# Optimization experiments

Hardware: AMD Instinct MI355X
Metric: run time of the kernel (lower is better)

Reference implementation:

```python
import jax, jax.numpy as jnp
import numpy as np

EPS = 1e-8

def rms_norm(x, scale):
    # norm(2,-1)/sqrt(d); x / (rms + eps) * scale
    d = x.shape[-1]
    norm = jnp.sqrt(jnp.sum(x * x, axis=-1, keepdims=True))
    rms = norm / jnp.sqrt(jnp.asarray(d, x.dtype))
    return scale * (x / (rms + EPS))

def setup_inputs() -> dict:
    key = jax.random.key(0)
    B, N, C, FF = 2, 2048, 1024, 4096
    ks = jax.random.split(key, 12)
    s = 0.02
    return {
        "x":  jax.random.normal(ks[0], (B, N, C), jnp.float32),
        "wq": jax.random.normal(ks[1], (C, C), jnp.float32) * s,
        "bq": jnp.zeros((C,), jnp.float32),
        "wk": jax.random.normal(ks[2], (C, C), jnp.float32) * s,
        "bk": jnp.zeros((C,), jnp.float32),
        "wv": jax.random.normal(ks[3], (C, C), jnp.float32) * s,
        "bv": jnp.zeros((C,), jnp.float32),
        "wo": jax.random.normal(ks[4], (C, C), jnp.float32) * s,
        "bo": jnp.zeros((C,), jnp.float32),
        "scale1": jnp.ones((C,), jnp.float32),
        "scale2": jnp.ones((C,), jnp.float32),
        "w1": jax.random.normal(ks[5], (C, FF), jnp.float32) * s,
        "b1": jnp.zeros((FF,), jnp.float32),
        "w2": jax.random.normal(ks[6], (FF, C), jnp.float32) * s,
        "b2": jnp.zeros((C,), jnp.float32),
    }

def reference(x, wq, bq, wk, bk, wv, bv, wo, bo, scale1, scale2, w1, b1, w2, b2):
    B, N, C = x.shape
    H = 16
    D = C // H

    residual = x
    xn = rms_norm(x, scale1)

    def heads(y):  # [B,N,C] -> [B,H,N,D]
        return y.reshape(B, N, H, D).transpose(0, 2, 1, 3)

    q = heads(xn @ wq + bq)
    k = heads(xn @ wk + bk)
    v = heads(xn @ wv + bv)

    # apply_rotary_pos_emb with cos=sin=1: q' = q - roll(q,1,-1), same for k
    q = q - jnp.roll(q, 1, axis=-1)
    k = k - jnp.roll(k, 1, axis=-1)

    # explicit attention (no causal mask in original)
    scores = jnp.einsum('bhnd,bhmd->bhnm', q, k) / jnp.sqrt(jnp.asarray(D, x.dtype))
    probs = jax.nn.softmax(scores, axis=-1)
    attn = jnp.einsum('bhnm,bhmd->bhnd', probs, v)
    attn = attn.transpose(0, 2, 1, 3).reshape(B, N, C)
    attn = attn @ wo + bo

    x = residual + attn
    residual = x
    xn = rms_norm(x, scale2)
    h = jax.nn.gelu(xn @ w1 + b1, approximate=False)  # torch GELU default = exact
    ffn_out = h @ w2 + b2
    return residual + ffn_out
```

## Files before the change

kernel.cpp:

```cpp
#include <hip/hip_runtime.h>
#include <hip/hip_bf16.h>
#include <math.h>

typedef unsigned short u16;
typedef short s16x8 __attribute__((ext_vector_type(8)));
typedef __bf16 bf16x8v __attribute__((ext_vector_type(8)));
typedef float f32x4 __attribute__((ext_vector_type(4)));
typedef unsigned short u16x4 __attribute__((ext_vector_type(4)));

struct Ptr4 { float* p[4]; };
struct TW4 { const float* w[4]; u16* o[4]; };

__device__ __forceinline__ u16 f2b(float f) {
    __hip_bfloat16 h = __float2bfloat16(f);
    return __builtin_bit_cast(u16, h);
}
__device__ __forceinline__ float b2f(u16 u) {
    __hip_bfloat16 h = __builtin_bit_cast(__hip_bfloat16, u);
    return __bfloat162float(h);
}

__device__ __forceinline__ f32x4 mfma16(s16x8 a, s16x8 b, f32x4 c) {
    return __builtin_amdgcn_mfma_f32_16x16x32_bf16(
        __builtin_bit_cast(bf16x8v, a), __builtin_bit_cast(bf16x8v, b), c, 0, 0, 0);
}

__device__ __forceinline__ void gl_lds16(const void* g, void* l) {
    typedef const unsigned int __attribute__((address_space(1))) * gp_t;
    typedef unsigned int __attribute__((address_space(3))) * lp_t;
    __builtin_amdgcn_global_load_lds((gp_t)(unsigned long long)g,
                                     (lp_t)(unsigned int)(unsigned long long)l,
                                     16, 0, 0);
}

__device__ __forceinline__ float gelu_fast(float v) {
    float u = 1.5957691216f * (v + 0.044715f * v * v * v);
    return v / (1.f + __expf(-u));
}

__global__ __launch_bounds__(256) void transpose_w(const float* __restrict__ W,
                                                   u16* __restrict__ Wt,
                                                   int K, int N) {
    __shared__ u16 tile[32][33];
    const int tx = threadIdx.x & 31, ty = threadIdx.x >> 5;
    const int n0 = blockIdx.x * 32, k0 = blockIdx.y * 32;
#pragma unroll
    for (int i = 0; i < 32; i += 8)
        tile[ty + i][tx] = f2b(W[(size_t)(k0 + ty + i) * N + n0 + tx]);
    __syncthreads();
#pragma unroll
    for (int i = 0; i < 32; i += 8)
        Wt[(size_t)(n0 + ty + i) * K + k0 + tx] = tile[tx][ty + i];
}

__global__ __launch_bounds__(256) void transpose_w4(TW4 io) {
    __shared__ u16 tile[32][33];
    const int z = blockIdx.z;
    const float* W = io.w[z];
    u16* Wt = io.o[z];
    const int tx = threadIdx.x & 31, ty = threadIdx.x >> 5;
    const int n0 = blockIdx.x * 32, k0 = blockIdx.y * 32;
#pragma unroll
    for (int i = 0; i < 32; i += 8)
        tile[ty + i][tx] = f2b(W[(size_t)(k0 + ty + i) * 1024 + n0 + tx]);
    __syncthreads();
#pragma unroll
    for (int i = 0; i < 32; i += 8)
        Wt[(size_t)(n0 + ty + i) * 1024 + k0 + tx] = tile[tx][ty + i];
}

__global__ __launch_bounds__(256) void transpose_v(const u16* __restrict__ qkv,
                                                   u16* __restrict__ vT) {
    __shared__ u16 tile[32][33];
    const int tx = threadIdx.x & 31, ty = threadIdx.x >> 5;
    const int n0 = blockIdx.x * 32, d0 = blockIdx.y * 32, bh = blockIdx.z;
    const int b = bh >> 4, h = bh & 15;
#pragma unroll
    for (int i = 0; i < 32; i += 8)
        tile[ty + i][tx] =
            qkv[(size_t)(b * 2048 + n0 + ty + i) * 3072 + 2048 + h * 64 + d0 + tx];
    __syncthreads();
#pragma unroll
    for (int i = 0; i < 32; i += 8)
        vT[((size_t)bh * 64 + d0 + ty + i) * 2048 + n0 + tx] = tile[tx][ty + i];
}

__global__ __launch_bounds__(256) void rmsnorm_kernel(const float* __restrict__ x,
                                                      const float* __restrict__ scale,
                                                      u16* __restrict__ out) {
    __shared__ float red[4];
    const int t = threadIdx.x, row = blockIdx.x;
    const float4* xr = (const float4*)(x + (size_t)row * 1024);
    float4 v = xr[t];
    float ss = v.x * v.x + v.y * v.y + v.z * v.z + v.w * v.w;
#pragma unroll
    for (int off = 1; off < 64; off <<= 1) ss += __shfl_xor(ss, off);
    if ((t & 63) == 0) red[t >> 6] = ss;
    __syncthreads();
    float tot = red[0] + red[1] + red[2] + red[3];
    float inv = 1.f / (sqrtf(tot * (1.f / 1024.f)) + 1e-8f);
    const float4* sr = (const float4*)scale;
    float4 s = sr[t];
    u16x4 o;
    o[0] = f2b(v.x * inv * s.x);
    o[1] = f2b(v.y * inv * s.y);
    o[2] = f2b(v.z * inv * s.z);
    o[3] = f2b(v.w * inv * s.w);
    ((u16x4*)(out + (size_t)row * 1024))[t] = o;
}

template <int EPI>
__global__ __launch_bounds__(256) void gemm_kernel(const u16* __restrict__ A,
                                                   const u16* __restrict__ Bt,
                                                   const float* __restrict__ bias,
                                                   const float* __restrict__ bias2,
                                                   const float* __restrict__ bias3,
                                                   const float* __restrict__ resid,
                                                   void* __restrict__ outp,
                                                   int M, int N, int K) {
    __shared__ __align__(16) u16 As[128 * 32];
    __shared__ __align__(16) u16 Bs[128 * 32];
    const int t = threadIdx.x, lane = t & 63;
    const int w = t >> 6, wm = (w >> 1) * 64, wn = (w & 1) * 64;
    const int c = lane & 15, qd = lane >> 4;
    const int n0 = blockIdx.x * 128, m0 = blockIdx.y * 128;

    const int sch = ((t & 3) ^ ((t >> 3) & 3)) * 8;
    const u16* Ag = A + (size_t)(m0 + (t >> 2)) * K + sch;
    const u16* Bg = Bt + (size_t)(n0 + (t >> 2)) * K + sch;
    const size_t half = (size_t)64 * K;
    const int fsw = ((c >> 1) & 3);

    f32x4 acc[4][4] = {};
    for (int kt = 0; kt < K; kt += 32) {
        __syncthreads();
        gl_lds16(Ag, &As[t * 8]);
        gl_lds16(Ag + half, &As[2048 + t * 8]);
        gl_lds16(Bg, &Bs[t * 8]);
        gl_lds16(Bg + half, &Bs[2048 + t * 8]);
        Ag += 32;
        Bg += 32;
        __syncthreads();
        s16x8 a[4], b[4];
#pragma unroll
        for (int im = 0; im < 4; im++)
            a[im] = *(const s16x8*)&As[(wm + im * 16 + c) * 32 + ((qd ^ fsw) * 8)];
#pragma unroll
        for (int jn = 0; jn < 4; jn++)
            b[jn] = *(const s16x8*)&Bs[(wn + jn * 16 + c) * 32 + ((qd ^ fsw) * 8)];
#pragma unroll
        for (int im = 0; im < 4; im++)
#pragma unroll
            for (int jn = 0; jn < 4; jn++)
                acc[im][jn] = mfma16(a[im], b[jn], acc[im][jn]);
    }

    if (EPI == 3) {
        const int colbase = n0 + wn;
        const bool isq = colbase < 1024, isv = colbase >= 2048;
        const float* bp = isq ? bias : (isv ? bias3 : bias2);
        const int cb = colbase & 1023;
#pragma unroll
        for (int im = 0; im < 4; im++)
#pragma unroll
            for (int r = 0; r < 4; r++) {
                float v[4], sh[4], b15[4];
#pragma unroll
                for (int jn = 0; jn < 4; jn++)
                    v[jn] = acc[im][jn][r] + bp[cb + jn * 16 + c];
#pragma unroll
                for (int jn = 0; jn < 4; jn++) {
                    sh[jn] = __shfl(v[jn], qd * 16 + ((c + 15) & 15));
                    b15[jn] = __shfl(v[jn], qd * 16 + 15);
                }
                const int rowg = m0 + wm + im * 16 + qd * 4 + r;
#pragma unroll
                for (int jn = 0; jn < 4; jn++) {
                    float prev = (c == 0) ? b15[(jn + 3) & 3] : sh[jn];
                    float ov = isv ? v[jn] : (v[jn] - prev);
                    if (isq) ov *= 0.125f;
                    ((u16*)outp)[(size_t)rowg * N + colbase + jn * 16 + c] = f2b(ov);
                }
            }
        return;
    }

#pragma unroll
    for (int im = 0; im < 4; im++) {
#pragma unroll
        for (int jn = 0; jn < 4; jn++) {
            const int colg = n0 + wn + jn * 16 + c;
            const float bv = bias[colg];
#pragma unroll
            for (int r = 0; r < 4; r++) {
                const int rowg = m0 + wm + im * 16 + qd * 4 + r;
                const size_t off = (size_t)rowg * N + colg;
                float v = acc[im][jn][r] + bv;
                if (EPI == 0) {
                    ((u16*)outp)[off] = f2b(v);
                } else if (EPI == 1) {
                    ((float*)outp)[off] = v + resid[off];
                } else {
                    ((u16*)outp)[off] = f2b(gelu_fast(v));
                }
            }
        }
    }
}

__global__ __launch_bounds__(256) void gemm_splitk(const u16* __restrict__ A,
                                                   const u16* __restrict__ Bt,
                                                   Ptr4 parts,
                                                   int N, int Ktot, int Kc) {
    __shared__ __align__(16) u16 As[128 * 32];
    __shared__ __align__(16) u16 Bs[128 * 32];
    const int t = threadIdx.x, lane = t & 63;
    const int w = t >> 6, wm = (w >> 1) * 64, wn = (w & 1) * 64;
    const int c = lane & 15, qd = lane >> 4;
    const int n0 = blockIdx.x * 128, m0 = blockIdx.y * 128;
    const int z = blockIdx.z;
    float* out = parts.p[z];

    const int sch = ((t & 3) ^ ((t >> 3) & 3)) * 8;
    const u16* Ag = A + (size_t)(m0 + (t >> 2)) * Ktot + z * Kc + sch;
    const u16* Bg = Bt + (size_t)(n0 + (t >> 2)) * Ktot + z * Kc + sch;
    const size_t half = (size_t)64 * Ktot;
    const int fsw = ((c >> 1) & 3);

    f32x4 acc[4][4] = {};
    for (int kt = 0; kt < Kc; kt += 32) {
        __syncthreads();
        gl_lds16(Ag, &As[t * 8]);
        gl_lds16(Ag + half, &As[2048 + t * 8]);
        gl_lds16(Bg, &Bs[t * 8]);
        gl_lds16(Bg + half, &Bs[2048 + t * 8]);
        Ag += 32;
        Bg += 32;
        __syncthreads();
        s16x8 a[4], b[4];
#pragma unroll
        for (int im = 0; im < 4; im++)
            a[im] = *(const s16x8*)&As[(wm + im * 16 + c) * 32 + ((qd ^ fsw) * 8)];
#pragma unroll
        for (int jn = 0; jn < 4; jn++)
            b[jn] = *(const s16x8*)&Bs[(wn + jn * 16 + c) * 32 + ((qd ^ fsw) * 8)];
#pragma unroll
        for (int im = 0; im < 4; im++)
#pragma unroll
            for (int jn = 0; jn < 4; jn++)
                acc[im][jn] = mfma16(a[im], b[jn], acc[im][jn]);
    }

#pragma unroll
    for (int im = 0; im < 4; im++)
#pragma unroll
        for (int jn = 0; jn < 4; jn++) {
            const int colg = n0 + wn + jn * 16 + c;
#pragma unroll
            for (int r = 0; r < 4; r++) {
                const int rowg = m0 + wm + im * 16 + qd * 4 + r;
                out[(size_t)rowg * N + colg] = acc[im][jn][r];
            }
        }
}

template <int S, bool NORM>
__global__ __launch_bounds__(256) void reduce_kernel(Ptr4 parts,
                                                     const float* __restrict__ bias,
                                                     const float* __restrict__ resid,
                                                     const float* __restrict__ scale,
                                                     float* __restrict__ yout,
                                                     u16* __restrict__ xnout) {
    __shared__ float red[4];
    const int t = threadIdx.x, row = blockIdx.x;
    const size_t base = (size_t)row * 1024;
    float4 v = ((const float4*)(resid + base))[t];
    float4 bv = ((const float4*)bias)[t];
    v.x += bv.x; v.y += bv.y; v.z += bv.z; v.w += bv.w;
#pragma unroll
    for (int s = 0; s < S; s++) {
        float4 pv = ((const float4*)(parts.p[s] + base))[t];
        v.x += pv.x; v.y += pv.y; v.z += pv.z; v.w += pv.w;
    }
    ((float4*)(yout + base))[t] = v;
    if (NORM) {
        float ss = v.x * v.x + v.y * v.y + v.z * v.z + v.w * v.w;
#pragma unroll
        for (int off = 1; off < 64; off <<= 1) ss += __shfl_xor(ss, off);
        if ((t & 63) == 0) red[t >> 6] = ss;
        __syncthreads();
        float tot = red[0] + red[1] + red[2] + red[3];
        float inv = 1.f / (sqrtf(tot * (1.f / 1024.f)) + 1e-8f);
        float4 s = ((const float4*)scale)[t];
        u16x4 o;
        o[0] = f2b(v.x * inv * s.x);
        o[1] = f2b(v.y * inv * s.y);
        o[2] = f2b(v.z * inv * s.z);
        o[3] = f2b(v.w * inv * s.w);
        ((u16x4*)(xnout + base))[t] = o;
    }
}

__global__ __launch_bounds__(256) void attn_kernel(const u16* __restrict__ qkv,
                                                   const u16* __restrict__ vT,
                                                   u16* __restrict__ attn) {
    __shared__ __align__(16) u16 Qs[64 * 64];
    __shared__ __align__(16) u16 Ks[2][64 * 64];
    __shared__ __align__(16) u16 Vs[2][64 * 64];
    __shared__ __align__(16) u16 Ps[4 * 16 * 64];

    const int t = threadIdx.x, lane = t & 63, w = t >> 6;
    const int c = lane & 15, qd = lane >> 4;
    const int bh = blockIdx.y, b = bh >> 4, h = bh & 15;
    const int q0 = blockIdx.x * 64;
    const size_t rowbase = (size_t)b * 2048;

    const u16* qg = qkv + (rowbase + q0) * 3072 + h * 64;
    const u16* kg = qkv + rowbase * 3072 + 1024 + h * 64;
    const u16* vg = vT + (size_t)bh * 64 * 2048;

    const int srow = t >> 3;
    const int sch = (t & 7) ^ (srow & 7);

    const u16* kptr = kg + (size_t)srow * 3072 + sch * 8;
    const u16* vptr = vg + (size_t)srow * 2048 + sch * 8;

    gl_lds16(qg + (size_t)srow * 3072 + sch * 8, &Qs[t * 8]);
    gl_lds16(qg + (size_t)(srow + 32) * 3072 + sch * 8, &Qs[2048 + t * 8]);
    gl_lds16(kptr, &Ks[0][t * 8]);
    gl_lds16(kptr + (size_t)32 * 3072, &Ks[0][2048 + t * 8]);
    gl_lds16(vptr, &Vs[0][t * 8]);
    gl_lds16(vptr + (size_t)32 * 2048, &Vs[0][2048 + t * 8]);
    __syncthreads();

    const int qrow = w * 16 + c;
    s16x8 qf[2];
#pragma unroll
    for (int ks = 0; ks < 2; ks++)
        qf[ks] = *(const s16x8*)&Qs[qrow * 64 + (((ks * 4 + qd) ^ (c & 7)) * 8)];

    float lsum[4] = {0.f, 0.f, 0.f, 0.f};
    f32x4 o[4] = {};
    u16* Pw = &Ps[w * 16 * 64];

    for (int it = 0; it < 32; it++) {
        const int buf = it & 1;
        const u16* Kb = Ks[buf];
        const u16* Vb = Vs[buf];

        s16x8 kf[2][4], vf[2][4];
#pragma unroll
        for (int ks = 0; ks < 2; ks++)
#pragma unroll
            for (int j = 0; j < 4; j++) {
                const int rrow = j * 16 + c;
                const int sw = ((ks * 4 + qd) ^ (rrow & 7)) * 8;
                kf[ks][j] = *(const s16x8*)&Kb[rrow * 64 + sw];
                vf[ks][j] = *(const s16x8*)&Vb[rrow * 64 + sw];
            }

        if (it + 1 < 32) {
            u16* Kn = Ks[buf ^ 1];
            u16* Vn = Vs[buf ^ 1];
            const size_t ko = (size_t)(it + 1) * 64 * 3072;
            const size_t vo = (size_t)(it + 1) * 64;
            gl_lds16(kptr + ko, &Kn[t * 8]);
            gl_lds16(kptr + ko + (size_t)32 * 3072, &Kn[2048 + t * 8]);
            gl_lds16(vptr + vo, &Vn[t * 8]);
            gl_lds16(vptr + vo + (size_t)32 * 2048, &Vn[2048 + t * 8]);
        }

        f32x4 sc[4] = {};
#pragma unroll
        for (int ks = 0; ks < 2; ks++)
#pragma unroll
            for (int jn = 0; jn < 4; jn++)
                sc[jn] = mfma16(qf[ks], kf[ks][jn], sc[jn]);

#pragma unroll
        for (int r = 0; r < 4; r++) {
            const int prow = qd * 4 + r;
            float s = 0.f;
#pragma unroll
            for (int jn = 0; jn < 4; jn++) {
                float p = __expf(sc[jn][r]);
                s += p;
                Pw[prow * 64 + (((jn * 2 + (c >> 3)) ^ (prow & 7)) * 8) + (c & 7)] =
                    f2b(p);
            }
            lsum[r] += s;
        }

#pragma unroll
        for (int ks = 0; ks < 2; ks++) {
            s16x8 pf = *(const s16x8*)&Pw[c * 64 + (((ks * 4 + qd) ^ (c & 7)) * 8)];
#pragma unroll
            for (int jd = 0; jd < 4; jd++)
                o[jd] = mfma16(pf, vf[ks][jd], o[jd]);
        }
        __syncthreads();
    }

#pragma unroll
    for (int r = 0; r < 4; r++)
#pragma unroll
        for (int off2 = 1; off2 < 16; off2 <<= 1)
            lsum[r] += __shfl_xor(lsum[r], off2);

    const int orow_base = b * 2048 + q0 + w * 16;
#pragma unroll
    for (int r = 0; r < 4; r++) {
        const float inv = 1.f / lsum[r];
        const int grow = orow_base + qd * 4 + r;
#pragma unroll
        for (int jd = 0; jd < 4; jd++)
            attn[(size_t)grow * 1024 + h * 64 + jd * 16 + c] = f2b(o[jd][r] * inv);
    }
}

extern "C" void kernel_launch(void* const* d_in, const int* in_sizes, int n_in,
                              void* d_out, int out_size, void* d_ws, size_t ws_size,
                              hipStream_t stream) {
    const float* x = (const float*)d_in[0];
    const float* wq = (const float*)d_in[1];
    const float* bq = (const float*)d_in[2];
    const float* wk = (const float*)d_in[3];
    const float* bk = (const float*)d_in[4];
    const float* wv = (const float*)d_in[5];
    const float* bv = (const float*)d_in[6];
    const float* wo = (const float*)d_in[7];
    const float* bo = (const float*)d_in[8];
    const float* scale1 = (const float*)d_in[9];
    const float* scale2 = (const float*)d_in[10];
    const float* w1 = (const float*)d_in[11];
    const float* b1 = (const float*)d_in[12];
    const float* w2 = (const float*)d_in[13];
    const float* b2 = (const float*)d_in[14];
    float* out = (float*)d_out;

    char* ws = (char*)d_ws;
    size_t off = 0;
    auto alloc = [&](size_t bytes) -> char* {
        char* p = ws + off;
        off += (bytes + 255) & ~(size_t)255;
        return p;
    };
    u16* wqkvT = (u16*)alloc((size_t)3072 * 1024 * 2);
    u16* woT   = (u16*)alloc((size_t)1024 * 1024 * 2);
    u16* w1T   = (u16*)alloc((size_t)4096 * 1024 * 2);
    u16* w2T   = (u16*)alloc((size_t)1024 * 4096 * 2);
    u16* xn    = (u16*)alloc((size_t)4096 * 1024 * 2);
    u16* qkv   = (u16*)alloc((size_t)4096 * 3072 * 2);
    u16* vT    = (u16*)alloc((size_t)32 * 64 * 2048 * 2);
    u16* attnb = (u16*)alloc((size_t)4096 * 1024 * 2);
    float* y1  = (float*)alloc((size_t)4096 * 1024 * 4);
    u16* hbuf  = (u16*)alloc((size_t)4096 * 4096 * 2);

    const size_t SPLIT = (size_t)4096 * 1024;
    Ptr4 po; po.p[0] = (float*)qkv; po.p[1] = (float*)qkv + SPLIT;
    po.p[2] = nullptr; po.p[3] = nullptr;
    Ptr4 pf; pf.p[0] = (float*)xn; pf.p[1] = (float*)xn + SPLIT;
    pf.p[2] = (float*)xn + 2 * SPLIT; pf.p[3] = (float*)wqkvT;

    dim3 blk(256);

    TW4 tw;
    tw.w[0] = wq; tw.o[0] = wqkvT;
    tw.w[1] = wk; tw.o[1] = wqkvT + (size_t)1024 * 1024;
    tw.w[2] = wv; tw.o[2] = wqkvT + (size_t)2048 * 1024;
    tw.w[3] = wo; tw.o[3] = woT;
    transpose_w4<<<dim3(32, 32, 4), blk, 0, stream>>>(tw);
    transpose_w<<<dim3(128, 32), blk, 0, stream>>>(w1, w1T, 1024, 4096);
    transpose_w<<<dim3(32, 128), blk, 0, stream>>>(w2, w2T, 4096, 1024);

    rmsnorm_kernel<<<4096, blk, 0, stream>>>(x, scale1, xn);
    gemm_kernel<3><<<dim3(24, 32), blk, 0, stream>>>(xn, wqkvT, bq, bk, bv, nullptr, qkv, 4096, 3072, 1024);
    transpose_v<<<dim3(64, 2, 32), blk, 0, stream>>>(qkv, vT);
    attn_kernel<<<dim3(32, 32), blk, 0, stream>>>(qkv, vT, attnb);
    gemm_splitk<<<dim3(8, 32, 2), blk, 0, stream>>>(attnb, woT, po, 1024, 1024, 512);
    reduce_kernel<2, true><<<4096, blk, 0, stream>>>(po, bo, x, scale2, y1, xn);
    gemm_kernel<2><<<dim3(32, 32), blk, 0, stream>>>(xn, w1T, b1, nullptr, nullptr, nullptr, hbuf, 4096, 4096, 1024);
    gemm_splitk<<<dim3(8, 32, 4), blk, 0, stream>>>(hbuf, w2T, pf, 1024, 4096, 1024);
    reduce_kernel<4, false><<<4096, blk, 0, stream>>>(pf, b2, y1, nullptr, out, nullptr);
}
```

Before: 411.6 us.

## Enlarge attention query tile to 128 rows so each K/V tile is reused twice

The attention kernel now processes 128 query rows per block instead of 64, with each wave handling two 16-row query sub-tiles against every K/V tile loaded into LDS. This halves the global K/V traffic and LDS fragment loads per query row. The K/V fragment reads are also moved after the next-tile prefetch is issued. The cost is a grid of 512 blocks instead of 1024, which is fewer than four waves' worth across the CUs, plus more registers and LDS per block, which may lower occupancy.

```diff
diff --git a/kernel.cpp b/kernel.cpp
--- a/kernel.cpp
+++ b/kernel.cpp
@@ -14,10 +14,6 @@
 __device__ __forceinline__ u16 f2b(float f) {
     __hip_bfloat16 h = __float2bfloat16(f);
     return __builtin_bit_cast(u16, h);
-}
-__device__ __forceinline__ float b2f(u16 u) {
-    __hip_bfloat16 h = __builtin_bit_cast(__hip_bfloat16, u);
-    return __bfloat162float(h);
 }
 
 __device__ __forceinline__ f32x4 mfma16(s16x8 a, s16x8 b, f32x4 c) {
@@ -304,15 +300,15 @@
 __global__ __launch_bounds__(256) void attn_kernel(const u16* __restrict__ qkv,
                                                    const u16* __restrict__ vT,
                                                    u16* __restrict__ attn) {
-    __shared__ __align__(16) u16 Qs[64 * 64];
+    __shared__ __align__(16) u16 Qs[128 * 64];
     __shared__ __align__(16) u16 Ks[2][64 * 64];
     __shared__ __align__(16) u16 Vs[2][64 * 64];
-    __shared__ __align__(16) u16 Ps[4 * 16 * 64];
+    __shared__ __align__(16) u16 Ps[4 * 32 * 64];
 
     const int t = threadIdx.x, lane = t & 63, w = t >> 6;
     const int c = lane & 15, qd = lane >> 4;
     const int bh = blockIdx.y, b = bh >> 4, h = bh & 15;
-    const int q0 = blockIdx.x * 64;
+    const int q0 = blockIdx.x * 128;
     const size_t rowbase = (size_t)b * 2048;
 
     const u16* qg = qkv + (rowbase + q0) * 3072 + h * 64;
@@ -325,39 +321,31 @@
     const u16* kptr = kg + (size_t)srow * 3072 + sch * 8;
     const u16* vptr = vg + (size_t)srow * 2048 + sch * 8;
 
-    gl_lds16(qg + (size_t)srow * 3072 + sch * 8, &Qs[t * 8]);
-    gl_lds16(qg + (size_t)(srow + 32) * 3072 + sch * 8, &Qs[2048 + t * 8]);
+#pragma unroll
+    for (int i = 0; i < 4; i++)
+        gl_lds16(qg + (size_t)(srow + i * 32) * 3072 + sch * 8, &Qs[t * 8 + i * 2048]);
     gl_lds16(kptr, &Ks[0][t * 8]);
     gl_lds16(kptr + (size_t)32 * 3072, &Ks[0][2048 + t * 8]);
     gl_lds16(vptr, &Vs[0][t * 8]);
     gl_lds16(vptr + (size_t)32 * 2048, &Vs[0][2048 + t * 8]);
     __syncthreads();
 
-    const int qrow = w * 16 + c;
-    s16x8 qf[2];
-#pragma unroll
-    for (int ks = 0; ks < 2; ks++)
-        qf[ks] = *(const s16x8*)&Qs[qrow * 64 + (((ks * 4 + qd) ^ (c & 7)) * 8)];
-
-    float lsum[4] = {0.f, 0.f, 0.f, 0.f};
-    f32x4 o[4] = {};
-    u16* Pw = &Ps[w * 16 * 64];
+    s16x8 qf[2][2];
+#pragma unroll
+    for (int im = 0; im < 2; im++)
+#pragma unroll
+        for (int ks = 0; ks < 2; ks++)
+            qf[im][ks] = *(const s16x8*)&Qs[(w * 32 + im * 16 + c) * 64 +
+                                            (((ks * 4 + qd) ^ (c & 7)) * 8)];
+
+    float lsum[2][4] = {};
+    f32x4 o[2][4] = {};
+    u16* Pw = &Ps[w * 32 * 64];
 
     for (int it = 0; it < 32; it++) {
         const int buf = it & 1;
         const u16* Kb = Ks[buf];
         const u16* Vb = Vs[buf];
-
-        s16x8 kf[2][4], vf[2][4];
-#pragma unroll
-        for (int ks = 0; ks < 2; ks++)
-#pragma unroll
-            for (int j = 0; j < 4; j++) {
-                const int rrow = j * 16 + c;
-                const int sw = ((ks * 4 + qd) ^ (rrow & 7)) * 8;
-                kf[ks][j] = *(const s16x8*)&Kb[rrow * 64 + sw];
-                vf[ks][j] = *(const s16x8*)&Vb[rrow * 64 + sw];
-            }
 
         if (it + 1 < 32) {
             u16* Kn = Ks[buf ^ 1];
@@ -370,52 +358,73 @@
             gl_lds16(vptr + vo + (size_t)32 * 2048, &Vn[2048 + t * 8]);
         }
 
-        f32x4 sc[4] = {};
+        s16x8 kf[2][4], vf[2][4];
 #pragma unroll
         for (int ks = 0; ks < 2; ks++)
 #pragma unroll
-            for (int jn = 0; jn < 4; jn++)
-                sc[jn] = mfma16(qf[ks], kf[ks][jn], sc[jn]);
-
+            for (int j = 0; j < 4; j++) {
+                const int rrow = j * 16 + c;
+                const int sw = ((ks * 4 + qd) ^ (rrow & 7)) * 8;
+                kf[ks][j] = *(const s16x8*)&Kb[rrow * 64 + sw];
+                vf[ks][j] = *(const s16x8*)&Vb[rrow * 64 + sw];
+            }
+
+#pragma unroll
+        for (int im = 0; im < 2; im++) {
+            f32x4 sc[4] = {};
+#pragma unroll
+            for (int ks = 0; ks < 2; ks++)
+#pragma unroll
+                for (int jn = 0; jn < 4; jn++)
+                    sc[jn] = mfma16(qf[im][ks], kf[ks][jn], sc[jn]);
+#pragma unroll
+            for (int r = 0; r < 4; r++) {
+                const int prow = im * 16 + qd * 4 + r;
+                float s = 0.f;
+#pragma unroll
+                for (int jn = 0; jn < 4; jn++) {
+                    float p = __expf(sc[jn][r]);
+                    s += p;
+                    Pw[prow * 64 + (((jn * 2 + (c >> 3)) ^ (prow & 7)) * 8) + (c & 7)] =
+                        f2b(p);
+                }
+                lsum[im][r] += s;
+            }
+        }
+
+#pragma unroll
+        for (int im = 0; im < 2; im++)
+#pragma unroll
+            for (int ks = 0; ks < 2; ks++) {
+                s16x8 pf = *(const s16x8*)&Pw[(im * 16 + c) * 64 +
+                                              (((ks * 4 + qd) ^ (c & 7)) * 8)];
+#pragma unroll
+                for (int jd = 0; jd < 4; jd++)
+                    o[im][jd] = mfma16(pf, vf[ks][jd], o[im][jd]);
+            }
+        __syncthreads();
+    }
+
+#pragma unroll
+    for (int im = 0; im < 2; im++)
+#pragma unroll
+        for (int r = 0; r < 4; r++)
+#pragma unroll
+            for (int off2 = 1; off2 < 16; off2 <<= 1)
+                lsum[im][r] += __shfl_xor(lsum[im][r], off2);
+
+    const int orow_base = b * 2048 + q0 + w * 32;
+#pragma unroll
+    for (int im = 0; im < 2; im++)
 #pragma unroll
         for (int r = 0; r < 4; r++) {
-            const int prow = qd * 4 + r;
-            float s = 0.f;
-#pragma unroll
-            for (int jn = 0; jn < 4; jn++) {
-                float p = __expf(sc[jn][r]);
-                s += p;
-                Pw[prow * 64 + (((jn * 2 + (c >> 3)) ^ (prow & 7)) * 8) + (c & 7)] =
-                    f2b(p);
-            }
-            lsum[r] += s;
+            const float inv = 1.f / lsum[im][r];
+            const int grow = orow_base + im * 16 + qd * 4 + r;
+#pragma unroll
+            for (int jd = 0; jd < 4; jd++)
+                attn[(size_t)grow * 1024 + h * 64 + jd * 16 + c] =
+                    f2b(o[im][jd][r] * inv);
         }
-
-#pragma unroll
-        for (int ks = 0; ks < 2; ks++) {
-            s16x8 pf = *(const s16x8*)&Pw[c * 64 + (((ks * 4 + qd) ^ (c & 7)) * 8)];
-#pragma unroll
-            for (int jd = 0; jd < 4; jd++)
-                o[jd] = mfma16(pf, vf[ks][jd], o[jd]);
-        }
-        __syncthreads();
-    }
-
-#pragma unroll
-    for (int r = 0; r < 4; r++)
-#pragma unroll
-        for (int off2 = 1; off2 < 16; off2 <<= 1)
-            lsum[r] += __shfl_xor(lsum[r], off2);
-
-    const int orow_base = b * 2048 + q0 + w * 16;
-#pragma unroll
-    for (int r = 0; r < 4; r++) {
-        const float inv = 1.f / lsum[r];
-        const int grow = orow_base + qd * 4 + r;
-#pragma unroll
-        for (int jd = 0; jd < 4; jd++)
-            attn[(size_t)grow * 1024 + h * 64 + jd * 16 + c] = f2b(o[jd][r] * inv);
-    }
 }
 
 extern "C" void kernel_launch(void* const* d_in, const int* in_sizes, int n_in,
@@ -476,7 +485,7 @@
     rmsnorm_kernel<<<4096, blk, 0, stream>>>(x, scale1, xn);
     gemm_kernel<3><<<dim3(24, 32), blk, 0, stream>>>(xn, wqkvT, bq, bk, bv, nullptr, qkv, 4096, 3072, 1024);
     transpose_v<<<dim3(64, 2, 32), blk, 0, stream>>>(qkv, vT);
-    attn_kernel<<<dim3(32, 32), blk, 0, stream>>>(qkv, vT, attnb);
+    attn_kernel<<<dim3(16, 32), blk, 0, stream>>>(qkv, vT, attnb);
     gemm_splitk<<<dim3(8, 32, 2), blk, 0, stream>>>(attnb, woT, po, 1024, 1024, 512);
     reduce_kernel<2, true><<<4096, blk, 0, stream>>>(po, bo, x, scale2, y1, xn);
     gemm_kernel<2><<<dim3(32, 32), blk, 0, stream>>>(xn, w1T, b1, nullptr, nullptr, nullptr, hbuf, 4096, 4096, 1024);
```

New measurement: 405.4 us. About the same (-1.5%).
